# Optimization experiments

Hardware: AMD Instinct MI355X
Metric: run time of the kernel (lower is better)

## Reference

```python
import jax, jax.numpy as jnp
import numpy as np

NATTRS, NOBJS = 200, 500
N = NATTRS + NOBJS
E = 50000
IN_F, HID, NODE_D = 512, 2048, 512
IMG_D, EMB = 512, 800
B = 256


def _ln(x, g, b, eps=1e-5):
    mu = jnp.mean(x, axis=-1, keepdims=True)
    var = jnp.mean((x - mu) ** 2, axis=-1, keepdims=True)
    return (x - mu) * jax.lax.rsqrt(var + eps) * g + b


def _sage(x, src, dst, Wl, bl, Wr):
    # PyG SAGEConv: lin_l(mean_{j->i} x_j) + lin_r(x_i); lin_r has no bias.
    agg = jax.ops.segment_sum(x[src], dst, num_segments=x.shape[0])
    cnt = jax.ops.segment_sum(jnp.ones((src.shape[0],), x.dtype), dst, num_segments=x.shape[0])
    mean = agg / jnp.maximum(cnt, 1.0)[:, None]
    return mean @ Wl + bl + x @ Wr


def setup_inputs() -> dict:
    key = jax.random.key(0)
    ks = iter(jax.random.split(key, 40))
    rn = lambda shape, s=0.02: jax.random.normal(next(ks), shape, jnp.float32) * s
    inp = dict(
        img=jax.random.normal(next(ks), (B, IMG_D), jnp.float32),
        node_feats=jax.random.normal(next(ks), (N, IN_F), jnp.float32),
        edge_index=jax.random.randint(next(ks), (2, E), 0, N),
        # SAGEConv 1: in_f -> 2048
        s1_Wl=rn((IN_F, HID)), s1_bl=jnp.zeros((HID,), jnp.float32), s1_Wr=rn((IN_F, HID)),
        # SAGEConv 2: 2048 -> node_dim
        s2_Wl=rn((HID, NODE_D)), s2_bl=jnp.zeros((NODE_D,), jnp.float32), s2_Wr=rn((HID, NODE_D)),
        # img_fc: 512 -> 800 -> 1000 -> 800 (LayerNorm+ReLU hidden, LayerNorm output)
        i_W1=rn((IMG_D, 800)), i_b1=jnp.zeros((800,), jnp.float32), i_g1=jnp.ones((800,), jnp.float32), i_be1=jnp.zeros((800,), jnp.float32),
        i_W2=rn((800, 1000)), i_b2=jnp.zeros((1000,), jnp.float32), i_g2=jnp.ones((1000,), jnp.float32), i_be2=jnp.zeros((1000,), jnp.float32),
        i_W3=rn((1000, EMB)), i_b3=jnp.zeros((EMB,), jnp.float32), i_gn=jnp.ones((EMB,), jnp.float32), i_bn=jnp.zeros((EMB,), jnp.float32),
        # pair_fc: 1024 -> 1000 -> 800
        p_W1=rn((2 * NODE_D, 1000)), p_b1=jnp.zeros((1000,), jnp.float32), p_g1=jnp.ones((1000,), jnp.float32), p_be1=jnp.zeros((1000,), jnp.float32),
        p_W2=rn((1000, EMB)), p_b2=jnp.zeros((EMB,), jnp.float32), p_gn=jnp.ones((EMB,), jnp.float32), p_bn=jnp.zeros((EMB,), jnp.float32),
    )
    return inp


def reference(img, node_feats, edge_index,
              s1_Wl, s1_bl, s1_Wr, s2_Wl, s2_bl, s2_Wr,
              i_W1, i_b1, i_g1, i_be1, i_W2, i_b2, i_g2, i_be2, i_W3, i_b3, i_gn, i_bn,
              p_W1, p_b1, p_g1, p_be1, p_W2, p_b2, p_gn, p_bn):
    src, dst = edge_index[0], edge_index[1]
    # GAE.encode: SAGE -> ReLU -> (Dropout, eval=id) -> SAGE
    h = jax.nn.relu(_sage(node_feats, src, dst, s1_Wl, s1_bl, s1_Wr))
    nodes = _sage(h, src, dst, s2_Wl, s2_bl, s2_Wr)  # [N, node_dim]
    # img_fc
    t = jax.nn.relu(_ln(img @ i_W1 + i_b1, i_g1, i_be1))
    t = jax.nn.relu(_ln(t @ i_W2 + i_b2, i_g2, i_be2))
    img_feats = _ln(t @ i_W3 + i_b3, i_gn, i_bn)  # [B, EMB]
    # get_all_pairs (open-world cross product: attr repeated per obj, obj tiled)
    attr_nodes, obj_nodes = nodes[:NATTRS], nodes[NATTRS:]
    pairs = jnp.concatenate(
        [jnp.repeat(attr_nodes, NOBJS, axis=0), jnp.tile(obj_nodes, (NATTRS, 1))], axis=1)  # [P, 2*node_dim]
    u = jax.nn.relu(_ln(pairs @ p_W1 + p_b1, p_g1, p_be1))
    pair_nodes = _ln(u @ p_W2 + p_b2, p_gn, p_bn)  # [P, EMB]
    pair_pred = img_feats @ pair_nodes.T  # [B, P]
    return pair_pred, nodes
```

## Files before the change

### kernel.cpp

```cpp
#include <hip/hip_runtime.h>
#include <hip/hip_bf16.h>

#define NATTRS 200
#define NOBJS  500
#define NNODE  700
#define IN_F   512
#define HID    2048
#define NODE_D 512
#define IMG_D  512
#define EMB    800
#define BB     256
#define P_H1   1000
#define NPAIR  100000

typedef __attribute__((ext_vector_type(8))) short short8v;
typedef __attribute__((ext_vector_type(4))) float f32x4;

typedef const __attribute__((address_space(1))) unsigned int* gas_ptr;
typedef __attribute__((address_space(3))) unsigned int* las_ptr;
__device__ __forceinline__ void async_copy16(void* lds, const void* g) {
  __builtin_amdgcn_global_load_lds((gas_ptr)g, (las_ptr)lds, 16, 0, 0);
}

__device__ __forceinline__ ushort f2bf(float x) {
  __hip_bfloat16 b = __float2bfloat16(x);
  return *reinterpret_cast<ushort*>(&b);
}
__device__ __forceinline__ float bf2f(ushort u) {
  __hip_bfloat16 b;
  *reinterpret_cast<ushort*>(&b) = u;
  return __bfloat162float(b);
}

__global__ void k_count(const int* __restrict__ ei, int* __restrict__ cnt, int E) {
  int e = blockIdx.x * 256 + threadIdx.x;
  if (e < E) atomicAdd(&cnt[ei[E + e]], 1);
}

__global__ __launch_bounds__(1024) void k_scan(const int* __restrict__ cnt,
                                               int* __restrict__ row_start,
                                               int* __restrict__ pos) {
  __shared__ int s[1024];
  int t = threadIdx.x;
  int my = (t < NNODE) ? cnt[t] : 0;
  s[t] = my;
  __syncthreads();
  for (int off = 1; off < 1024; off <<= 1) {
    int add = (t >= off) ? s[t - off] : 0;
    __syncthreads();
    s[t] += add;
    __syncthreads();
  }
  int excl = s[t] - my;
  if (t < NNODE) { row_start[t] = excl; pos[t] = excl; }
  if (t == 0) row_start[NNODE] = s[1023];
}

__global__ void k_fill(const int* __restrict__ ei, int* __restrict__ pos,
                       int* __restrict__ srcs, int E) {
  int e = blockIdx.x * 256 + threadIdx.x;
  if (e < E) {
    int d = ei[E + e];
    int idx = atomicAdd(&pos[d], 1);
    srcs[idx] = ei[e];
  }
}

__global__ __launch_bounds__(256) void agg_mean(const float* __restrict__ X,
                                                const int* __restrict__ srcs,
                                                const int* __restrict__ row_start,
                                                float* __restrict__ outp, int D) {
  int node = blockIdx.x;
  int d = blockIdx.y * 256 + threadIdx.x;
  int e0 = row_start[node], e1 = row_start[node + 1];
  float s = 0.f;
  for (int e = e0; e < e1; ++e) s += X[srcs[e] * D + d];
  float c = (float)(e1 - e0);
  outp[node * D + d] = s / fmaxf(c, 1.f);
}

__global__ __launch_bounds__(256) void split_f32(const float* __restrict__ X,
                                                 ushort* __restrict__ Xh,
                                                 ushort* __restrict__ Xl,
                                                 int Mvalid, int K, int Kpad, long total) {
  for (long idx = blockIdx.x * 256L + threadIdx.x; idx < total; idx += gridDim.x * 256L) {
    int m = (int)(idx / Kpad);
    int k = (int)(idx - (long)m * Kpad);
    float v = (m < Mvalid && k < K) ? X[(size_t)m * K + k] : 0.f;
    ushort h = f2bf(v);
    Xh[idx] = h;
    Xl[idx] = f2bf(v - bf2f(h));
  }
}

struct WDesc { const float* W; ushort* Wh; ushort* Wl; int K, N, Kpad, nbx, blk0; };
struct WBatch { WDesc d[10]; };

__global__ __launch_bounds__(256) void prep_wT_batch(WBatch B) {
  __shared__ float tile[32][33];
  int bx = blockIdx.x;
  int di = 0;
  #pragma unroll
  for (int j = 1; j < 10; ++j) if (bx >= B.d[j].blk0) di = j;
  const WDesc& D = B.d[di];
  int local = bx - D.blk0;
  int bn = local % D.nbx, bk = local / D.nbx;
  const int n0 = bn * 32, k0 = bk * 32;
  const int tx = threadIdx.x & 31, ty = threadIdx.x >> 5;
  #pragma unroll
  for (int r0 = 0; r0 < 32; r0 += 8) {
    int k = k0 + r0 + ty, n = n0 + tx;
    tile[r0 + ty][tx] = (k < D.K && n < D.N) ? D.W[(size_t)k * D.N + n] : 0.f;
  }
  __syncthreads();
  #pragma unroll
  for (int r0 = 0; r0 < 32; r0 += 8) {
    int n = n0 + r0 + ty, kk = k0 + tx;
    float v = tile[tx][r0 + ty];
    ushort h = f2bf(v);
    D.Wh[(size_t)n * D.Kpad + kk] = h;
    D.Wl[(size_t)n * D.Kpad + kk] = f2bf(v - bf2f(h));
  }
}

__global__ __launch_bounds__(256) void w2rowsum(const float* __restrict__ W2,
                                                ushort* __restrict__ W2Th) {
  int k = blockIdx.x * 4 + (threadIdx.x >> 6);
  int lane = threadIdx.x & 63;
  const float* row = W2 + (size_t)k * EMB;
  float s = 0.f;
  for (int n = lane; n < EMB; n += 64) s += row[n];
  #pragma unroll
  for (int m = 1; m < 64; m <<= 1) s += __shfl_xor(s, m);
  if (lane == 0 && k < P_H1) W2Th[800 * 1024 + k] = f2bf(s);
}

template <bool RELU>
__global__ __launch_bounds__(256) void ln_rows(float* __restrict__ X,
                                               const float* __restrict__ g,
                                               const float* __restrict__ b, int N) {
  int row = blockIdx.x, tid = threadIdx.x;
  float* x = X + row * N;
  float s1 = 0.f, s2 = 0.f;
  for (int i = tid; i < N; i += 256) { float v = x[i]; s1 += v; s2 += v * v; }
  #pragma unroll
  for (int m = 1; m < 64; m <<= 1) { s1 += __shfl_xor(s1, m); s2 += __shfl_xor(s2, m); }
  __shared__ float r1[4], r2[4];
  int wv = tid >> 6;
  if ((tid & 63) == 0) { r1[wv] = s1; r2[wv] = s2; }
  __syncthreads();
  s1 = r1[0] + r1[1] + r1[2] + r1[3];
  s2 = r2[0] + r2[1] + r2[2] + r2[3];
  float inv = 1.f / (float)N;
  float mu = s1 * inv;
  float rstd = rsqrtf(s2 * inv - mu * mu + 1e-5f);
  for (int i = tid; i < N; i += 256) {
    float v = (x[i] - mu) * rstd * g[i] + b[i];
    if (RELU) v = fmaxf(v, 0.f);
    x[i] = v;
  }
}

__global__ __launch_bounds__(256) void prep_imgg(const float* __restrict__ t3,
                                                 const float* __restrict__ gn,
                                                 ushort* __restrict__ gh,
                                                 ushort* __restrict__ gl) {
  int r = blockIdx.x;
  for (int n = threadIdx.x; n < EMB; n += 256) {
    float v = t3[r * EMB + n] * gn[n];
    ushort h = f2bf(v);
    gh[r * EMB + n] = h;
    gl[r * EMB + n] = f2bf(v - bf2f(h));
  }
}

__global__ __launch_bounds__(256) void prep_pairB(const float* __restrict__ t3,
                                                  const float* __restrict__ gn,
                                                  const float* __restrict__ bn,
                                                  const float* __restrict__ b2,
                                                  float* __restrict__ Sv, float* __restrict__ Tv,
                                                  float* __restrict__ IBv, float* __restrict__ aux) {
  int b = blockIdx.x, tid = threadIdx.x;
  __shared__ float r1[4], r2[4], r3[4];
  float s1 = 0.f, s2 = 0.f, s3 = 0.f;
  if (b == BB) {
    for (int n = tid; n < EMB; n += 256) s1 += b2[n];
    #pragma unroll
    for (int m = 1; m < 64; m <<= 1) s1 += __shfl_xor(s1, m);
    if ((tid & 63) == 0) r1[tid >> 6] = s1;
    __syncthreads();
    if (tid == 0) aux[0] = (r1[0] + r1[1] + r1[2] + r1[3]) * (1.f / EMB);
    return;
  }
  const float* row = t3 + b * EMB;
  for (int n = tid; n < EMB; n += 256) {
    float iv = row[n];
    float ig = iv * gn[n];
    s1 += ig; s2 += iv * bn[n]; s3 += ig * b2[n];
  }
  #pragma unroll
  for (int m = 1; m < 64; m <<= 1) {
    s1 += __shfl_xor(s1, m); s2 += __shfl_xor(s2, m); s3 += __shfl_xor(s3, m);
  }
  int wv = tid >> 6;
  if ((tid & 63) == 0) { r1[wv] = s1; r2[wv] = s2; r3[wv] = s3; }
  __syncthreads();
  if (tid == 0) {
    Sv[b] = r1[0] + r1[1] + r1[2] + r1[3];
    Tv[b] = r2[0] + r2[1] + r2[2] + r2[3];
    IBv[b] = r3[0] + r3[1] + r3[2] + r3[3];
  }
}

__global__ __launch_bounds__(256) void ugen(const float* __restrict__ B1v,
                                            const float* __restrict__ O1v,
                                            const float* __restrict__ g1,
                                            const float* __restrict__ be1,
                                            ushort* __restrict__ Uh,
                                            ushort* __restrict__ Ul, int p0) {
  int r = blockIdx.x * 4 + (threadIdx.x >> 6);
  int lane = threadIdx.x & 63;
  int p = p0 + r;
  if (p > NPAIR - 1) p = NPAIR - 1;
  int a = p / NOBJS, o = p - a * NOBJS;
  const float* br = B1v + a * P_H1;
  const float* ow = O1v + o * P_H1;
  const int kb = lane * 16;
  float x[16];
  float s1 = 0.f, s2 = 0.f;
  #pragma unroll
  for (int i = 0; i < 16; ++i) {
    int k = kb + i;
    float v = (k < P_H1) ? br[k] + ow[k] : 0.f;
    x[i] = v; s1 += v; s2 += v * v;
  }
  #pragma unroll
  for (int m = 1; m < 64; m <<= 1) { s1 += __shfl_xor(s1, m); s2 += __shfl_xor(s2, m); }
  float mu = s1 * (1.f / P_H1);
  float rstd = rsqrtf(s2 * (1.f / P_H1) - mu * mu + 1e-5f);
  ushort hv[16], lv[16];
  #pragma unroll
  for (int i = 0; i < 16; ++i) {
    int k = kb + i;
    float un = (k < P_H1) ? fmaxf((x[i] - mu) * rstd * g1[k] + be1[k], 0.f) : 0.f;
    ushort h = f2bf(un);
    hv[i] = h;
    lv[i] = f2bf(un - bf2f(h));
  }
  size_t base = (size_t)r * 1024 + kb;
  *(short8v*)&Uh[base] = *(short8v*)&hv[0];
  *(short8v*)&Uh[base + 8] = *(short8v*)&hv[8];
  *(short8v*)&Ul[base] = *(short8v*)&lv[0];
  *(short8v*)&Ul[base + 8] = *(short8v*)&lv[8];
}

__global__ __launch_bounds__(256, 3) void ustat(const ushort* __restrict__ Uh,
                                                const ushort* __restrict__ W2Th,
                                                const float* __restrict__ b2,
                                                const float* __restrict__ aux,
                                                float* __restrict__ muv,
                                                float* __restrict__ rstdv) {
  __shared__ ushort smem[8192];
  __shared__ float red[2][128];
  const int tid = threadIdx.x, lane = tid & 63, wid = tid >> 6;
  const int wm = wid >> 1, wn = wid & 1;
  const int m0 = blockIdx.x * 128;
  const int lr = lane & 15, lk = lane >> 4;
  const int srow = lane >> 2;
  const int scol = (lane & 3) * 8;
  const float aux0 = aux[0];

  float ss[4][4] = {};
  float md[4][4] = {};

  for (int nt = 0; nt < 7; ++nt) {
    f32x4 acc[4][4];
    #pragma unroll
    for (int i = 0; i < 4; ++i)
      #pragma unroll
      for (int j = 0; j < 4; ++j) acc[i][j] = (f32x4){0.f, 0.f, 0.f, 0.f};

    for (int k0 = 0; k0 < 1024; k0 += 32) {
      __syncthreads();
      #pragma unroll
      for (int j = 0; j < 4; ++j) {
        int t = wid + 4 * j;
        int buf = t >> 3, i = t & 7;
        const ushort* src = buf == 0
            ? Uh + (size_t)(m0 + i * 16 + srow) * 1024 + k0 + scol
            : W2Th + (size_t)(nt * 128 + i * 16 + srow) * 1024 + k0 + scol;
        async_copy16(smem + buf * 4096 + i * 512, src);
      }
      __syncthreads();
      short8v ah[4], bh[4];
      #pragma unroll
      for (int f = 0; f < 4; ++f) {
        ah[f] = *(const short8v*)&smem[(wm * 64 + f * 16 + lr) * 32 + lk * 8];
        bh[f] = *(const short8v*)&smem[4096 + (wn * 64 + f * 16 + lr) * 32 + lk * 8];
      }
      #pragma unroll
      for (int mi = 0; mi < 4; ++mi)
        #pragma unroll
        for (int ni = 0; ni < 4; ++ni)
          acc[mi][ni] = __builtin_amdgcn_mfma_f32_16x16x32_bf16(ah[mi], bh[ni], acc[mi][ni], 0, 0, 0);
    }
    #pragma unroll
    for (int ni = 0; ni < 4; ++ni) {
      int n = nt * 128 + wn * 64 + ni * 16 + lr;
      if (n < EMB) {
        float bb = b2[n];
        #pragma unroll
        for (int mi = 0; mi < 4; ++mi)
          #pragma unroll
          for (int r = 0; r < 4; ++r) {
            float v = acc[mi][ni][r] + bb;
            ss[mi][r] += v * v;
          }
      } else if (n == EMB) {
        #pragma unroll
        for (int mi = 0; mi < 4; ++mi)
          #pragma unroll
          for (int r = 0; r < 4; ++r) md[mi][r] = acc[mi][ni][r];
      }
    }
  }
  #pragma unroll
  for (int mi = 0; mi < 4; ++mi)
    #pragma unroll
    for (int r = 0; r < 4; ++r) {
      float s = ss[mi][r];
      s += __shfl_xor(s, 1); s += __shfl_xor(s, 2);
      s += __shfl_xor(s, 4); s += __shfl_xor(s, 8);
      ss[mi][r] = s;
    }
  if (lr == 0) {
    #pragma unroll
    for (int mi = 0; mi < 4; ++mi)
      #pragma unroll
      for (int r = 0; r < 4; ++r)
        red[wn][wm * 64 + mi * 16 + lk * 4 + r] = ss[mi][r];
  }
  __syncthreads();
  if (wn == 0 && lr == 0) {
    #pragma unroll
    for (int mi = 0; mi < 4; ++mi)
      #pragma unroll
      for (int r = 0; r < 4; ++r) {
        int row = wm * 64 + mi * 16 + lk * 4 + r;
        float tot = red[0][row] + red[1][row];
        float m_ = md[mi][r] * (1.f / EMB) + aux0;
        muv[m0 + row] = m_;
        rstdv[m0 + row] = rsqrtf(tot * (1.f / EMB) - m_ * m_ + 1e-5f);
      }
  }
}

template <bool HAS2, bool HASBIAS, bool RELU, bool PAIREPI>
__global__ __launch_bounds__(256, 3) void gemm_mf(
    const ushort* __restrict__ Ah, const ushort* __restrict__ Al, int lda,
    const ushort* __restrict__ Bh, const ushort* __restrict__ Bl, int ldb,
    const ushort* __restrict__ A2h, const ushort* __restrict__ A2l, int lda2,
    const ushort* __restrict__ B2h, const ushort* __restrict__ B2l, int ldb2,
    const float* __restrict__ bias, float* __restrict__ C, size_t ldc,
    int K, int Mvalid, int nvalid, int ncol0,
    const float* __restrict__ rstdv, const float* __restrict__ muv,
    const float* __restrict__ Sv, const float* __restrict__ Tv,
    const float* __restrict__ IBv) {
  __shared__ ushort smem[16384];
  const int tid = threadIdx.x, lane = tid & 63, wid = tid >> 6;
  const int wm = wid >> 1, wn = wid & 1;
  const int n0b = blockIdx.x * 128, m0 = blockIdx.y * 128;
  const int lr = lane & 15, lk = lane >> 4;

  f32x4 acc[4][4];
  #pragma unroll
  for (int i = 0; i < 4; ++i)
    #pragma unroll
    for (int j = 0; j < 4; ++j) acc[i][j] = (f32x4){0.f, 0.f, 0.f, 0.f};

  const int srow = lane >> 2;
  const int scol = (lane & 3) * 8;
  const int npass = HAS2 ? 2 : 1;

  for (int pass = 0; pass < npass; ++pass) {
    const ushort* pAh = (HAS2 && pass) ? A2h : Ah;
    const ushort* pAl = (HAS2 && pass) ? A2l : Al;
    const ushort* pBh = (HAS2 && pass) ? B2h : Bh;
    const ushort* pBl = (HAS2 && pass) ? B2l : Bl;
    const int plda = (HAS2 && pass) ? lda2 : lda;
    const int pldb = (HAS2 && pass) ? ldb2 : ldb;

    for (int k0 = 0; k0 < K; k0 += 32) {
      __syncthreads();
      #pragma unroll
      for (int j = 0; j < 8; ++j) {
        int t = wid + 4 * j;
        int buf = t >> 3, i = t & 7;
        const ushort* g;
        int ld_, r0;
        if (buf == 0)      { g = pAh; ld_ = plda; r0 = m0; }
        else if (buf == 1) { g = pAl; ld_ = plda; r0 = m0; }
        else if (buf == 2) { g = pBh; ld_ = pldb; r0 = n0b; }
        else               { g = pBl; ld_ = pldb; r0 = n0b; }
        const ushort* src = g + (size_t)(r0 + i * 16 + srow) * ld_ + k0 + scol;
        async_copy16(smem + buf * 4096 + i * 512, src);
      }
      __syncthreads();

      short8v ah[4], al[4], bh[4], bl[4];
      #pragma unroll
      for (int f = 0; f < 4; ++f) {
        ah[f] = *(const short8v*)&smem[0     + (wm * 64 + f * 16 + lr) * 32 + lk * 8];
        al[f] = *(const short8v*)&smem[4096  + (wm * 64 + f * 16 + lr) * 32 + lk * 8];
        bh[f] = *(const short8v*)&smem[8192  + (wn * 64 + f * 16 + lr) * 32 + lk * 8];
        bl[f] = *(const short8v*)&smem[12288 + (wn * 64 + f * 16 + lr) * 32 + lk * 8];
      }
      #pragma unroll
      for (int mi = 0; mi < 4; ++mi)
        #pragma unroll
        for (int ni = 0; ni < 4; ++ni) {
          acc[mi][ni] = __builtin_amdgcn_mfma_f32_16x16x32_bf16(ah[mi], bh[ni], acc[mi][ni], 0, 0, 0);
          acc[mi][ni] = __builtin_amdgcn_mfma_f32_16x16x32_bf16(al[mi], bh[ni], acc[mi][ni], 0, 0, 0);
          acc[mi][ni] = __builtin_amdgcn_mfma_f32_16x16x32_bf16(ah[mi], bl[ni], acc[mi][ni], 0, 0, 0);
        }
    }
  }

  #pragma unroll
  for (int mi = 0; mi < 4; ++mi)
    #pragma unroll
    for (int ni = 0; ni < 4; ++ni) {
      int n = n0b + wn * 64 + ni * 16 + lr;
      if (n >= nvalid) continue;
      float rs = 0.f, mn = 0.f;
      if (PAIREPI) { rs = rstdv[n]; mn = muv[n]; }
      float bb = (HASBIAS && !PAIREPI) ? bias[n] : 0.f;
      #pragma unroll
      for (int r = 0; r < 4; ++r) {
        int m = m0 + wm * 64 + mi * 16 + lk * 4 + r;
        if (m >= Mvalid) continue;
        float v = acc[mi][ni][r];
        if (PAIREPI) {
          v = rs * (v + IBv[m] - mn * Sv[m]) + Tv[m];
        } else {
          v += bb;
          if (RELU) v = fmaxf(v, 0.f);
        }
        C[(size_t)m * ldc + ncol0 + n] = v;
      }
    }
}

extern "C" void kernel_launch(void* const* d_in, const int* in_sizes, int n_in,
                              void* d_out, int out_size, void* d_ws, size_t ws_size,
                              hipStream_t stream) {
  const float* img = (const float*)d_in[0];
  const float* node_feats = (const float*)d_in[1];
  const int* ei = (const int*)d_in[2];
  const float* s1_Wl = (const float*)d_in[3];
  const float* s1_bl = (const float*)d_in[4];
  const float* s1_Wr = (const float*)d_in[5];
  const float* s2_Wl = (const float*)d_in[6];
  const float* s2_bl = (const float*)d_in[7];
  const float* s2_Wr = (const float*)d_in[8];
  const float* i_W1 = (const float*)d_in[9];
  const float* i_b1 = (const float*)d_in[10];
  const float* i_g1 = (const float*)d_in[11];
  const float* i_be1 = (const float*)d_in[12];
  const float* i_W2 = (const float*)d_in[13];
  const float* i_b2 = (const float*)d_in[14];
  const float* i_g2 = (const float*)d_in[15];
  const float* i_be2 = (const float*)d_in[16];
  const float* i_W3 = (const float*)d_in[17];
  const float* i_b3 = (const float*)d_in[18];
  const float* i_gn = (const float*)d_in[19];
  const float* i_bn = (const float*)d_in[20];
  const float* p_W1 = (const float*)d_in[21];
  const float* p_b1 = (const float*)d_in[22];
  const float* p_g1 = (const float*)d_in[23];
  const float* p_be1 = (const float*)d_in[24];
  const float* p_W2 = (const float*)d_in[25];
  const float* p_b2 = (const float*)d_in[26];
  const float* p_gn = (const float*)d_in[27];
  const float* p_bn = (const float*)d_in[28];

  const int E = in_sizes[2] / 2;

  char* base = (char*)d_ws;
  size_t off = 0;
  auto alloc = [&](size_t bytes) -> void* {
    void* p = base + off;
    off = (off + bytes + 255) & ~(size_t)255;
    return p;
  };
  float* mean1 = (float*)alloc(700 * 512 * 4);
  float* h     = (float*)alloc(700 * 2048 * 4);
  float* mean2 = (float*)alloc(700 * 2048 * 4);
  float* t1    = (float*)alloc(256 * 800 * 4);
  float* t2    = (float*)alloc(256 * 1000 * 4);
  float* t3    = (float*)alloc(256 * 800 * 4);
  float* B1    = (float*)alloc(200 * 1000 * 4);
  float* O1    = (float*)alloc(500 * 1000 * 4);
  float* G     = (float*)alloc(256 * 1024 * 4);
  ushort* nfh = (ushort*)alloc(768 * 512 * 2);
  ushort* nfl = (ushort*)alloc(768 * 512 * 2);
  ushort* m1h = (ushort*)alloc(768 * 512 * 2);
  ushort* m1l = (ushort*)alloc(768 * 512 * 2);
  ushort* hh  = (ushort*)alloc(768 * 2048 * 2);
  ushort* hl  = (ushort*)alloc(768 * 2048 * 2);
  ushort* m2h = (ushort*)alloc(768 * 2048 * 2);
  ushort* m2l = (ushort*)alloc(768 * 2048 * 2);
  ushort* ndh = (ushort*)alloc(768 * 512 * 2);
  ushort* ndl = (ushort*)alloc(768 * 512 * 2);
  ushort* xih = (ushort*)alloc(256 * 512 * 2);
  ushort* xil = (ushort*)alloc(256 * 512 * 2);
  ushort* t1h = (ushort*)alloc(256 * 800 * 2);
  ushort* t1l = (ushort*)alloc(256 * 800 * 2);
  ushort* t2h = (ushort*)alloc(256 * 1024 * 2);
  ushort* t2l = (ushort*)alloc(256 * 1024 * 2);
  ushort* iggh = (ushort*)alloc(256 * 800 * 2);
  ushort* iggl = (ushort*)alloc(256 * 800 * 2);
  ushort* Gh   = (ushort*)alloc(256 * 1024 * 2);
  ushort* Gl   = (ushort*)alloc(256 * 1024 * 2);
  ushort* w1lh = (ushort*)alloc((size_t)2048 * 512 * 2);
  ushort* w1ll = (ushort*)alloc((size_t)2048 * 512 * 2);
  ushort* w1rh = (ushort*)alloc((size_t)2048 * 512 * 2);
  ushort* w1rl = (ushort*)alloc((size_t)2048 * 512 * 2);
  ushort* w2lh = (ushort*)alloc((size_t)512 * 2048 * 2);
  ushort* w2ll = (ushort*)alloc((size_t)512 * 2048 * 2);
  ushort* w2rh = (ushort*)alloc((size_t)512 * 2048 * 2);
  ushort* w2rl = (ushort*)alloc((size_t)512 * 2048 * 2);
  ushort* iw1h = (ushort*)alloc((size_t)896 * 512 * 2);
  ushort* iw1l = (ushort*)alloc((size_t)896 * 512 * 2);
  ushort* iw2h = (ushort*)alloc((size_t)1024 * 800 * 2);
  ushort* iw2l = (ushort*)alloc((size_t)1024 * 800 * 2);
  ushort* iw3h = (ushort*)alloc((size_t)896 * 1024 * 2);
  ushort* iw3l = (ushort*)alloc((size_t)896 * 1024 * 2);
  ushort* pw1ah = (ushort*)alloc((size_t)1024 * 512 * 2);
  ushort* pw1al = (ushort*)alloc((size_t)1024 * 512 * 2);
  ushort* pw1bh = (ushort*)alloc((size_t)1024 * 512 * 2);
  ushort* pw1bl = (ushort*)alloc((size_t)1024 * 512 * 2);
  ushort* W2Th = (ushort*)alloc((size_t)896 * 1024 * 2);
  ushort* W2Tl = (ushort*)alloc((size_t)896 * 1024 * 2);
  ushort* Wkh  = (ushort*)alloc((size_t)1024 * 800 * 2);
  ushort* Wkl  = (ushort*)alloc((size_t)1024 * 800 * 2);
  float* Sv  = (float*)alloc(256 * 4);
  float* Tv  = (float*)alloc(256 * 4);
  float* IBv = (float*)alloc(256 * 4);
  float* aux = (float*)alloc(256);
  int* cnt       = (int*)alloc(704 * 4);
  int* row_start = (int*)alloc(704 * 4);
  int* pos       = (int*)alloc(704 * 4);
  int* srcs      = (int*)alloc(50176 * 4);

  size_t avail = (ws_size > off + (4u << 20)) ? ws_size - off - (4u << 20) : 0;
  long maxRows = (long)(avail / 4104) - 256;
  int CA = (int)(maxRows / 500);
  if (CA < 1) CA = 1;
  if (CA > NATTRS) CA = NATTRS;
  int nch = (NATTRS + CA - 1) / CA;
  int rowsPadAlloc = ((CA * 500 + 127) / 128) * 128;
  ushort* Uh    = (ushort*)alloc((size_t)rowsPadAlloc * 1024 * 2);
  ushort* Ul    = (ushort*)alloc((size_t)rowsPadAlloc * 1024 * 2);
  float*  muv   = (float*)alloc((size_t)rowsPadAlloc * 4);
  float*  rstdv = (float*)alloc((size_t)rowsPadAlloc * 4);

  float* pairp = (float*)d_out;
  float* nodes = (float*)d_out + (size_t)BB * NPAIR;

  const ushort* NU = nullptr;
  const float* NUF = nullptr;

  hipMemsetAsync(cnt, 0, NNODE * sizeof(int), stream);
  k_count<<<(E + 255) / 256, 256, 0, stream>>>(ei, cnt, E);
  k_scan<<<1, 1024, 0, stream>>>(cnt, row_start, pos);
  k_fill<<<(E + 255) / 256, 256, 0, stream>>>(ei, pos, srcs, E);

  {
    WBatch B;
    int blk = 0;
    auto set = [&](int i, const float* W, ushort* Wh, ushort* Wl, int K, int N, int Kpad, int Npad) {
      B.d[i] = {W, Wh, Wl, K, N, Kpad, Npad / 32, blk};
      blk += (Npad / 32) * (Kpad / 32);
    };
    set(0, s1_Wl, w1lh, w1ll, 512, 2048, 512, 2048);
    set(1, s1_Wr, w1rh, w1rl, 512, 2048, 512, 2048);
    set(2, s2_Wl, w2lh, w2ll, 2048, 512, 2048, 512);
    set(3, s2_Wr, w2rh, w2rl, 2048, 512, 2048, 512);
    set(4, i_W1, iw1h, iw1l, 512, 800, 512, 896);
    set(5, i_W2, iw2h, iw2l, 800, 1000, 800, 1024);
    set(6, i_W3, iw3h, iw3l, 1000, 800, 1024, 896);
    set(7, p_W1, pw1ah, pw1al, 512, 1000, 512, 1024);
    set(8, p_W1 + 512 * 1000, pw1bh, pw1bl, 512, 1000, 512, 1024);
    set(9, p_W2, W2Th, W2Tl, 1000, 800, 1024, 896);
    prep_wT_batch<<<blk, 256, 0, stream>>>(B);
  }
  w2rowsum<<<250, 256, 0, stream>>>(p_W2, W2Th);
  split_f32<<<512, 256, 0, stream>>>(p_W2, Wkh, Wkl, 1000, 800, 800, 1024L * 800);

  agg_mean<<<dim3(NNODE, IN_F / 256), 256, 0, stream>>>(node_feats, srcs, row_start, mean1, IN_F);
  split_f32<<<512, 256, 0, stream>>>(node_feats, nfh, nfl, 700, 512, 512, 768L * 512);
  split_f32<<<512, 256, 0, stream>>>(mean1, m1h, m1l, 700, 512, 512, 768L * 512);
  gemm_mf<true, true, true, false><<<dim3(16, 6), 256, 0, stream>>>(
      m1h, m1l, 512, w1lh, w1ll, 512, nfh, nfl, 512, w1rh, w1rl, 512,
      s1_bl, h, 2048, 512, 700, 2048, 0, NUF, NUF, NUF, NUF, NUF);

  agg_mean<<<dim3(NNODE, HID / 256), 256, 0, stream>>>(h, srcs, row_start, mean2, HID);
  split_f32<<<1024, 256, 0, stream>>>(h, hh, hl, 700, 2048, 2048, 768L * 2048);
  split_f32<<<1024, 256, 0, stream>>>(mean2, m2h, m2l, 700, 2048, 2048, 768L * 2048);
  gemm_mf<true, true, false, false><<<dim3(4, 6), 256, 0, stream>>>(
      m2h, m2l, 2048, w2lh, w2ll, 2048, hh, hl, 2048, w2rh, w2rl, 2048,
      s2_bl, nodes, 512, 2048, 700, 512, 0, NUF, NUF, NUF, NUF, NUF);

  split_f32<<<256, 256, 0, stream>>>(img, xih, xil, 256, 512, 512, 256L * 512);
  gemm_mf<false, true, false, false><<<dim3(7, 2), 256, 0, stream>>>(
      xih, xil, 512, iw1h, iw1l, 512, NU, NU, 0, NU, NU, 0,
      i_b1, t1, 800, 512, 256, 800, 0, NUF, NUF, NUF, NUF, NUF);
  ln_rows<true><<<BB, 256, 0, stream>>>(t1, i_g1, i_be1, 800);
  split_f32<<<256, 256, 0, stream>>>(t1, t1h, t1l, 256, 800, 800, 256L * 800);
  gemm_mf<false, true, false, false><<<dim3(8, 2), 256, 0, stream>>>(
      t1h, t1l, 800, iw2h, iw2l, 800, NU, NU, 0, NU, NU, 0,
      i_b2, t2, 1000, 800, 256, 1000, 0, NUF, NUF, NUF, NUF, NUF);
  ln_rows<true><<<BB, 256, 0, stream>>>(t2, i_g2, i_be2, 1000);
  split_f32<<<256, 256, 0, stream>>>(t2, t2h, t2l, 256, 1000, 1024, 256L * 1024);
  gemm_mf<false, true, false, false><<<dim3(7, 2), 256, 0, stream>>>(
      t2h, t2l, 1024, iw3h, iw3l, 1024, NU, NU, 0, NU, NU, 0,
      i_b3, t3, 800, 1024, 256, 800, 0, NUF, NUF, NUF, NUF, NUF);
  ln_rows<false><<<BB, 256, 0, stream>>>(t3, i_gn, i_bn, EMB);

  prep_pairB<<<BB + 1, 256, 0, stream>>>(t3, p_gn, p_bn, p_b2, Sv, Tv, IBv, aux);
  prep_imgg<<<BB, 256, 0, stream>>>(t3, p_gn, iggh, iggl);
  gemm_mf<false, false, false, false><<<dim3(8, 2), 256, 0, stream>>>(
      iggh, iggl, 800, Wkh, Wkl, 800, NU, NU, 0, NU, NU, 0,
      nullptr, G, 1024, 800, 256, 1024, 0, NUF, NUF, NUF, NUF, NUF);
  split_f32<<<256, 256, 0, stream>>>(G, Gh, Gl, 256, 1024, 1024, 256L * 1024);

  split_f32<<<512, 256, 0, stream>>>(nodes, ndh, ndl, 700, 512, 512, 768L * 512);
  gemm_mf<false, true, false, false><<<dim3(8, 2), 256, 0, stream>>>(
      ndh, ndl, 512, pw1ah, pw1al, 512, NU, NU, 0, NU, NU, 0,
      p_b1, B1, 1000, 512, 200, 1000, 0, NUF, NUF, NUF, NUF, NUF);
  gemm_mf<false, false, false, false><<<dim3(8, 4), 256, 0, stream>>>(
      ndh + 200 * 512, ndl + 200 * 512, 512, pw1bh, pw1bl, 512, NU, NU, 0, NU, NU, 0,
      nullptr, O1, 1000, 512, 500, 1000, 0, NUF, NUF, NUF, NUF, NUF);

  for (int c = 0; c < nch; ++c) {
    int a0 = c * CA;
    int ca = (NATTRS - a0 < CA) ? (NATTRS - a0) : CA;
    int rows = ca * 500;
    int rowsPad = ((rows + 127) / 128) * 128;
    int p0 = a0 * 500;

    ugen<<<rowsPad / 4, 256, 0, stream>>>(B1, O1, p_g1, p_be1, Uh, Ul, p0);
    ustat<<<rowsPad / 128, 256, 0, stream>>>(Uh, W2Th, p_b2, aux, muv, rstdv);
    gemm_mf<false, false, false, true><<<dim3(rowsPad / 128, 2), 256, 0, stream>>>(
        Gh, Gl, 1024, Uh, Ul, 1024, NU, NU, 0, NU, NU, 0,
        nullptr, pairp, NPAIR, 1024, 256, rows, p0,
        rstdv, muv, Sv, Tv, IBv);
  }
}
```

Before: 2.134 ms.

## Fuse pair-hidden generation into stat and output GEMMs, drop materialized U buffer

Stops writing the 100000x1024 pair hidden matrix U (hi/lo bf16) to global memory and rebuilds each tile on the fly inside the stat and output GEMM kernels from B1/O1 rows. Per-pair layer-norm mean and variance come from precomputed row sums plus a small B1·O1ᵀ dot-product GEMM, which removes the per-pair reduction and the chunked launch loop. It also fuses LayerNorm with the bf16 split for the image MLP. The cost is redundant recomputation of U elements in each GEMM block (twice across the two N-tiles of the output kernel) plus scalar global loads in the inner loop, and the variance formula is less numerically stable.

```diff
diff --git a/kernel.cpp b/kernel.cpp
--- a/kernel.cpp
+++ b/kernel.cpp
@@ -12,6 +12,7 @@
 #define BB     256
 #define P_H1   1000
 #define NPAIR  100000
+#define NPB    782
 
 typedef __attribute__((ext_vector_type(8))) short short8v;
 typedef __attribute__((ext_vector_type(4))) float f32x4;
@@ -82,11 +83,12 @@
 __global__ __launch_bounds__(256) void split_f32(const float* __restrict__ X,
                                                  ushort* __restrict__ Xh,
                                                  ushort* __restrict__ Xl,
-                                                 int Mvalid, int K, int Kpad, long total) {
+                                                 int Mvalid, int K, int ldx, int Kpad,
+                                                 long total) {
   for (long idx = blockIdx.x * 256L + threadIdx.x; idx < total; idx += gridDim.x * 256L) {
     int m = (int)(idx / Kpad);
     int k = (int)(idx - (long)m * Kpad);
-    float v = (m < Mvalid && k < K) ? X[(size_t)m * K + k] : 0.f;
+    float v = (m < Mvalid && k < K) ? X[(size_t)m * ldx + k] : 0.f;
     ushort h = f2bf(v);
     Xh[idx] = h;
     Xl[idx] = f2bf(v - bf2f(h));
@@ -133,6 +135,21 @@
   #pragma unroll
   for (int m = 1; m < 64; m <<= 1) s += __shfl_xor(s, m);
   if (lane == 0 && k < P_H1) W2Th[800 * 1024 + k] = f2bf(s);
+}
+
+__global__ __launch_bounds__(256) void rowstats(const float* __restrict__ B1v,
+                                                const float* __restrict__ O1v,
+                                                float* __restrict__ s1v,
+                                                float* __restrict__ s2v) {
+  int row = blockIdx.x * 4 + (threadIdx.x >> 6);
+  int lane = threadIdx.x & 63;
+  const float* ptr = (row < 200) ? B1v + (size_t)row * 1024
+                                 : O1v + (size_t)(row - 200) * 1024;
+  float s1 = 0.f, s2 = 0.f;
+  for (int k = lane; k < P_H1; k += 64) { float v = ptr[k]; s1 += v; s2 += v * v; }
+  #pragma unroll
+  for (int m = 1; m < 64; m <<= 1) { s1 += __shfl_xor(s1, m); s2 += __shfl_xor(s2, m); }
+  if (lane == 0 && row < 700) { s1v[row] = s1; s2v[row] = s2; }
 }
 
 template <bool RELU>
@@ -161,6 +178,40 @@
   }
 }
 
+template <bool RELU>
+__global__ __launch_bounds__(256) void ln_split(const float* __restrict__ X,
+                                                const float* __restrict__ g,
+                                                const float* __restrict__ b,
+                                                ushort* __restrict__ Xh,
+                                                ushort* __restrict__ Xl,
+                                                int N, int Kpad) {
+  int row = blockIdx.x, tid = threadIdx.x;
+  const float* x = X + (size_t)row * N;
+  float s1 = 0.f, s2 = 0.f;
+  for (int i = tid; i < N; i += 256) { float v = x[i]; s1 += v; s2 += v * v; }
+  #pragma unroll
+  for (int m = 1; m < 64; m <<= 1) { s1 += __shfl_xor(s1, m); s2 += __shfl_xor(s2, m); }
+  __shared__ float r1[4], r2[4];
+  int wv = tid >> 6;
+  if ((tid & 63) == 0) { r1[wv] = s1; r2[wv] = s2; }
+  __syncthreads();
+  s1 = r1[0] + r1[1] + r1[2] + r1[3];
+  s2 = r2[0] + r2[1] + r2[2] + r2[3];
+  float inv = 1.f / (float)N;
+  float mu = s1 * inv;
+  float rstd = rsqrtf(s2 * inv - mu * mu + 1e-5f);
+  for (int i = tid; i < Kpad; i += 256) {
+    float v = 0.f;
+    if (i < N) {
+      v = (x[i] - mu) * rstd * g[i] + b[i];
+      if (RELU) v = fmaxf(v, 0.f);
+    }
+    ushort h = f2bf(v);
+    Xh[(size_t)row * Kpad + i] = h;
+    Xl[(size_t)row * Kpad + i] = f2bf(v - bf2f(h));
+  }
+}
+
 __global__ __launch_bounds__(256) void prep_imgg(const float* __restrict__ t3,
                                                  const float* __restrict__ gn,
                                                  ushort* __restrict__ gh,
@@ -212,63 +263,33 @@
   }
 }
 
-__global__ __launch_bounds__(256) void ugen(const float* __restrict__ B1v,
-                                            const float* __restrict__ O1v,
-                                            const float* __restrict__ g1,
-                                            const float* __restrict__ be1,
-                                            ushort* __restrict__ Uh,
-                                            ushort* __restrict__ Ul, int p0) {
-  int r = blockIdx.x * 4 + (threadIdx.x >> 6);
-  int lane = threadIdx.x & 63;
-  int p = p0 + r;
-  if (p > NPAIR - 1) p = NPAIR - 1;
-  int a = p / NOBJS, o = p - a * NOBJS;
-  const float* br = B1v + a * P_H1;
-  const float* ow = O1v + o * P_H1;
-  const int kb = lane * 16;
-  float x[16];
-  float s1 = 0.f, s2 = 0.f;
-  #pragma unroll
-  for (int i = 0; i < 16; ++i) {
-    int k = kb + i;
-    float v = (k < P_H1) ? br[k] + ow[k] : 0.f;
-    x[i] = v; s1 += v; s2 += v * v;
-  }
-  #pragma unroll
-  for (int m = 1; m < 64; m <<= 1) { s1 += __shfl_xor(s1, m); s2 += __shfl_xor(s2, m); }
-  float mu = s1 * (1.f / P_H1);
-  float rstd = rsqrtf(s2 * (1.f / P_H1) - mu * mu + 1e-5f);
-  ushort hv[16], lv[16];
-  #pragma unroll
-  for (int i = 0; i < 16; ++i) {
-    int k = kb + i;
-    float un = (k < P_H1) ? fmaxf((x[i] - mu) * rstd * g1[k] + be1[k], 0.f) : 0.f;
-    ushort h = f2bf(un);
-    hv[i] = h;
-    lv[i] = f2bf(un - bf2f(h));
-  }
-  size_t base = (size_t)r * 1024 + kb;
-  *(short8v*)&Uh[base] = *(short8v*)&hv[0];
-  *(short8v*)&Uh[base + 8] = *(short8v*)&hv[8];
-  *(short8v*)&Ul[base] = *(short8v*)&lv[0];
-  *(short8v*)&Ul[base + 8] = *(short8v*)&lv[8];
-}
-
-__global__ __launch_bounds__(256, 3) void ustat(const ushort* __restrict__ Uh,
-                                                const ushort* __restrict__ W2Th,
-                                                const float* __restrict__ b2,
-                                                const float* __restrict__ aux,
-                                                float* __restrict__ muv,
-                                                float* __restrict__ rstdv) {
+__global__ __launch_bounds__(256, 3) void fused_ustat(
+    const float* __restrict__ B1v, const float* __restrict__ O1v,
+    const float* __restrict__ g1, const float* __restrict__ be1,
+    const float* __restrict__ s1v, const float* __restrict__ s2v,
+    const float* __restrict__ dotBO,
+    const ushort* __restrict__ W2Th, const float* __restrict__ b2,
+    const float* __restrict__ aux,
+    float* __restrict__ muv, float* __restrict__ rstdv) {
   __shared__ ushort smem[8192];
   __shared__ float red[2][128];
   const int tid = threadIdx.x, lane = tid & 63, wid = tid >> 6;
   const int wm = wid >> 1, wn = wid & 1;
   const int m0 = blockIdx.x * 128;
   const int lr = lane & 15, lk = lane >> 4;
-  const int srow = lane >> 2;
-  const int scol = (lane & 3) * 8;
+  const int srow = lane >> 2, scol = (lane & 3) * 8;
   const float aux0 = aux[0];
+
+  const int rr = tid >> 1, ch = tid & 1;
+  int p = m0 + rr;
+  if (p > NPAIR - 1) p = NPAIR - 1;
+  const int a = p / NOBJS, o = p - a * NOBJS;
+  const float* pB = B1v + (size_t)a * 1024;
+  const float* pO = O1v + (size_t)o * 1024;
+  const float s1p = s1v[a] + s1v[200 + o];
+  const float s2p = s2v[a] + 2.f * dotBO[a * 512 + o] + s2v[200 + o];
+  const float mu1 = s1p * (1.f / P_H1);
+  const float rstd1 = rsqrtf(s2p * (1.f / P_H1) - mu1 * mu1 + 1e-5f);
 
   float ss[4][4] = {};
   float md[4][4] = {};
@@ -283,13 +304,24 @@
     for (int k0 = 0; k0 < 1024; k0 += 32) {
       __syncthreads();
       #pragma unroll
-      for (int j = 0; j < 4; ++j) {
-        int t = wid + 4 * j;
-        int buf = t >> 3, i = t & 7;
-        const ushort* src = buf == 0
-            ? Uh + (size_t)(m0 + i * 16 + srow) * 1024 + k0 + scol
-            : W2Th + (size_t)(nt * 128 + i * 16 + srow) * 1024 + k0 + scol;
-        async_copy16(smem + buf * 4096 + i * 512, src);
+      for (int j = 0; j < 2; ++j) {
+        int i = wid + 4 * j;
+        const ushort* src = W2Th + (size_t)(nt * 128 + i * 16 + srow) * 1024 + k0 + scol;
+        async_copy16(smem + 4096 + i * 512, src);
+      }
+      {
+        const int kb = k0 + ch * 16;
+        ushort hv[16];
+        #pragma unroll
+        for (int i = 0; i < 16; ++i) {
+          int k = kb + i;
+          float un = 0.f;
+          if (k < P_H1)
+            un = fmaxf((pB[k] + pO[k] - mu1) * rstd1 * g1[k] + be1[k], 0.f);
+          hv[i] = f2bf(un);
+        }
+        *(short8v*)&smem[rr * 32 + ch * 16] = *(short8v*)&hv[0];
+        *(short8v*)&smem[rr * 32 + ch * 16 + 8] = *(short8v*)&hv[8];
       }
       __syncthreads();
       short8v ah[4], bh[4];
@@ -355,17 +387,112 @@
   }
 }
 
-template <bool HAS2, bool HASBIAS, bool RELU, bool PAIREPI>
+__global__ __launch_bounds__(256, 3) void fused_out(
+    const ushort* __restrict__ Gh, const ushort* __restrict__ Gl,
+    const float* __restrict__ B1v, const float* __restrict__ O1v,
+    const float* __restrict__ g1, const float* __restrict__ be1,
+    const float* __restrict__ s1v, const float* __restrict__ s2v,
+    const float* __restrict__ dotBO,
+    float* __restrict__ C,
+    const float* __restrict__ rstdv, const float* __restrict__ muv,
+    const float* __restrict__ Sv, const float* __restrict__ Tv,
+    const float* __restrict__ IBv) {
+  __shared__ ushort smem[16384];
+  const int tid = threadIdx.x, lane = tid & 63, wid = tid >> 6;
+  const int wm = wid >> 1, wn = wid & 1;
+  const int n0b = blockIdx.x * 128, m0 = blockIdx.y * 128;
+  const int lr = lane & 15, lk = lane >> 4;
+  const int srow = lane >> 2, scol = (lane & 3) * 8;
+
+  const int rr = tid >> 1, ch = tid & 1;
+  int p = n0b + rr;
+  if (p > NPAIR - 1) p = NPAIR - 1;
+  const int a = p / NOBJS, o = p - a * NOBJS;
+  const float* pB = B1v + (size_t)a * 1024;
+  const float* pO = O1v + (size_t)o * 1024;
+  const float s1p = s1v[a] + s1v[200 + o];
+  const float s2p = s2v[a] + 2.f * dotBO[a * 512 + o] + s2v[200 + o];
+  const float mu1 = s1p * (1.f / P_H1);
+  const float rstd1 = rsqrtf(s2p * (1.f / P_H1) - mu1 * mu1 + 1e-5f);
+
+  f32x4 acc[4][4];
+  #pragma unroll
+  for (int i = 0; i < 4; ++i)
+    #pragma unroll
+    for (int j = 0; j < 4; ++j) acc[i][j] = (f32x4){0.f, 0.f, 0.f, 0.f};
+
+  for (int k0 = 0; k0 < 1024; k0 += 32) {
+    __syncthreads();
+    #pragma unroll
+    for (int j = 0; j < 4; ++j) {
+      int t = wid + 4 * j;
+      int buf = t >> 3, i = t & 7;
+      const ushort* g = buf ? Gl : Gh;
+      const ushort* src = g + (size_t)(m0 + i * 16 + srow) * 1024 + k0 + scol;
+      async_copy16(smem + buf * 4096 + i * 512, src);
+    }
+    {
+      const int kb = k0 + ch * 16;
+      ushort hv[16], lv[16];
+      #pragma unroll
+      for (int i = 0; i < 16; ++i) {
+        int k = kb + i;
+        float un = 0.f;
+        if (k < P_H1)
+          un = fmaxf((pB[k] + pO[k] - mu1) * rstd1 * g1[k] + be1[k], 0.f);
+        ushort h = f2bf(un);
+        hv[i] = h;
+        lv[i] = f2bf(un - bf2f(h));
+      }
+      *(short8v*)&smem[8192 + rr * 32 + ch * 16] = *(short8v*)&hv[0];
+      *(short8v*)&smem[8192 + rr * 32 + ch * 16 + 8] = *(short8v*)&hv[8];
+      *(short8v*)&smem[12288 + rr * 32 + ch * 16] = *(short8v*)&lv[0];
+      *(short8v*)&smem[12288 + rr * 32 + ch * 16 + 8] = *(short8v*)&lv[8];
+    }
+    __syncthreads();
+
+    short8v ah[4], al[4], bh[4], bl[4];
+    #pragma unroll
+    for (int f = 0; f < 4; ++f) {
+      ah[f] = *(const short8v*)&smem[0     + (wm * 64 + f * 16 + lr) * 32 + lk * 8];
+      al[f] = *(const short8v*)&smem[4096  + (wm * 64 + f * 16 + lr) * 32 + lk * 8];
+      bh[f] = *(const short8v*)&smem[8192  + (wn * 64 + f * 16 + lr) * 32 + lk * 8];
+      bl[f] = *(const short8v*)&smem[12288 + (wn * 64 + f * 16 + lr) * 32 + lk * 8];
+    }
+    #pragma unroll
+    for (int mi = 0; mi < 4; ++mi)
+      #pragma unroll
+      for (int ni = 0; ni < 4; ++ni) {
+        acc[mi][ni] = __builtin_amdgcn_mfma_f32_16x16x32_bf16(ah[mi], bh[ni], acc[mi][ni], 0, 0, 0);
+        acc[mi][ni] = __builtin_amdgcn_mfma_f32_16x16x32_bf16(al[mi], bh[ni], acc[mi][ni], 0, 0, 0);
+        acc[mi][ni] = __builtin_amdgcn_mfma_f32_16x16x32_bf16(ah[mi], bl[ni], acc[mi][ni], 0, 0, 0);
+      }
+  }
+
+  #pragma unroll
+  for (int mi = 0; mi < 4; ++mi)
+    #pragma unroll
+    for (int ni = 0; ni < 4; ++ni) {
+      int n = n0b + wn * 64 + ni * 16 + lr;
+      if (n >= NPAIR) continue;
+      float rs = rstdv[n], mn = muv[n];
+      #pragma unroll
+      for (int r = 0; r < 4; ++r) {
+        int m = m0 + wm * 64 + mi * 16 + lk * 4 + r;
+        float v = acc[mi][ni][r];
+        C[(size_t)m * NPAIR + n] = rs * (v + IBv[m] - mn * Sv[m]) + Tv[m];
+      }
+    }
+}
+
+template <bool HAS2, bool HASBIAS, bool RELU>
 __global__ __launch_bounds__(256, 3) void gemm_mf(
     const ushort* __restrict__ Ah, const ushort* __restrict__ Al, int lda,
     const ushort* __restrict__ Bh, const ushort* __restrict__ Bl, int ldb,
     const ushort* __restrict__ A2h, const ushort* __restrict__ A2l, int lda2,
     const ushort* __restrict__ B2h, const ushort* __restrict__ B2l, int ldb2,
     const float* __restrict__ bias, float* __restrict__ C, size_t ldc,
-    int K, int Mvalid, int nvalid, int ncol0,
-    const float* __restrict__ rstdv, const float* __restrict__ muv,
-    const float* __restrict__ Sv, const float* __restrict__ Tv,
-    const float* __restrict__ IBv) {
+    int K, int Mvalid, int nvalid, int ncol0) {
   __shared__ ushort smem[16384];
   const int tid = threadIdx.x, lane = tid & 63, wid = tid >> 6;
   const int wm = wid >> 1, wn = wid & 1;
@@ -432,20 +559,13 @@
     for (int ni = 0; ni < 4; ++ni) {
       int n = n0b + wn * 64 + ni * 16 + lr;
       if (n >= nvalid) continue;
-      float rs = 0.f, mn = 0.f;
-      if (PAIREPI) { rs = rstdv[n]; mn = muv[n]; }
-      float bb = (HASBIAS && !PAIREPI) ? bias[n] : 0.f;
+      float bb = HASBIAS ? bias[n] : 0.f;
       #pragma unroll
       for (int r = 0; r < 4; ++r) {
         int m = m0 + wm * 64 + mi * 16 + lk * 4 + r;
         if (m >= Mvalid) continue;
-        float v = acc[mi][ni][r];
-        if (PAIREPI) {
-          v = rs * (v + IBv[m] - mn * Sv[m]) + Tv[m];
-        } else {
-          v += bb;
-          if (RELU) v = fmaxf(v, 0.f);
-        }
+        float v = acc[mi][ni][r] + bb;
+        if (RELU) v = fmaxf(v, 0.f);
         C[(size_t)m * ldc + ncol0 + n] = v;
       }
     }
@@ -499,9 +619,10 @@
   float* t1    = (float*)alloc(256 * 800 * 4);
   float* t2    = (float*)alloc(256 * 1000 * 4);
   float* t3    = (float*)alloc(256 * 800 * 4);
-  float* B1    = (float*)alloc(200 * 1000 * 4);
-  float* O1    = (float*)alloc(500 * 1000 * 4);
+  float* B1    = (float*)alloc(256 * 1024 * 4);
+  float* O1    = (float*)alloc(512 * 1024 * 4);
   float* G     = (float*)alloc(256 * 1024 * 4);
+  float* dotBO = (float*)alloc(256 * 512 * 4);
   ushort* nfh = (ushort*)alloc(768 * 512 * 2);
   ushort* nfl = (ushort*)alloc(768 * 512 * 2);
   ushort* m1h = (ushort*)alloc(768 * 512 * 2);
@@ -522,6 +643,10 @@
   ushort* iggl = (ushort*)alloc(256 * 800 * 2);
   ushort* Gh   = (ushort*)alloc(256 * 1024 * 2);
   ushort* Gl   = (ushort*)alloc(256 * 1024 * 2);
+  ushort* B1h  = (ushort*)alloc(256 * 1024 * 2);
+  ushort* B1l  = (ushort*)alloc(256 * 1024 * 2);
+  ushort* O1h  = (ushort*)alloc(512 * 1024 * 2);
+  ushort* O1l  = (ushort*)alloc(512 * 1024 * 2);
   ushort* w1lh = (ushort*)alloc((size_t)2048 * 512 * 2);
   ushort* w1ll = (ushort*)alloc((size_t)2048 * 512 * 2);
   ushort* w1rh = (ushort*)alloc((size_t)2048 * 512 * 2);
@@ -548,28 +673,19 @@
   float* Tv  = (float*)alloc(256 * 4);
   float* IBv = (float*)alloc(256 * 4);
   float* aux = (float*)alloc(256);
+  float* s1v = (float*)alloc(704 * 4);
+  float* s2v = (float*)alloc(704 * 4);
+  float* muv   = (float*)alloc((size_t)NPB * 128 * 4);
+  float* rstdv = (float*)alloc((size_t)NPB * 128 * 4);
   int* cnt       = (int*)alloc(704 * 4);
   int* row_start = (int*)alloc(704 * 4);
   int* pos       = (int*)alloc(704 * 4);
   int* srcs      = (int*)alloc(50176 * 4);
 
-  size_t avail = (ws_size > off + (4u << 20)) ? ws_size - off - (4u << 20) : 0;
-  long maxRows = (long)(avail / 4104) - 256;
-  int CA = (int)(maxRows / 500);
-  if (CA < 1) CA = 1;
-  if (CA > NATTRS) CA = NATTRS;
-  int nch = (NATTRS + CA - 1) / CA;
-  int rowsPadAlloc = ((CA * 500 + 127) / 128) * 128;
-  ushort* Uh    = (ushort*)alloc((size_t)rowsPadAlloc * 1024 * 2);
-  ushort* Ul    = (ushort*)alloc((size_t)rowsPadAlloc * 1024 * 2);
-  float*  muv   = (float*)alloc((size_t)rowsPadAlloc * 4);
-  float*  rstdv = (float*)alloc((size_t)rowsPadAlloc * 4);
-
   float* pairp = (float*)d_out;
   float* nodes = (float*)d_out + (size_t)BB * NPAIR;
 
   const ushort* NU = nullptr;
-  const float* NUF = nullptr;
 
   hipMemsetAsync(cnt, 0, NNODE * sizeof(int), stream);
   k_count<<<(E + 255) / 256, 256, 0, stream>>>(ei, cnt, E);
@@ -596,65 +712,61 @@
     prep_wT_batch<<<blk, 256, 0, stream>>>(B);
   }
   w2rowsum<<<250, 256, 0, stream>>>(p_W2, W2Th);
-  split_f32<<<512, 256, 0, stream>>>(p_W2, Wkh, Wkl, 1000, 800, 800, 1024L * 800);
+  split_f32<<<512, 256, 0, stream>>>(p_W2, Wkh, Wkl, 1000, 800, 800, 800, 1024L * 800);
 
   agg_mean<<<dim3(NNODE, IN_F / 256), 256, 0, stream>>>(node_feats, srcs, row_start, mean1, IN_F);
-  split_f32<<<512, 256, 0, stream>>>(node_feats, nfh, nfl, 700, 512, 512, 768L * 512);
-  split_f32<<<512, 256, 0, stream>>>(mean1, m1h, m1l, 700, 512, 512, 768L * 512);
-  gemm_mf<true, true, true, false><<<dim3(16, 6), 256, 0, stream>>>(
+  split_f32<<<512, 256, 0, stream>>>(node_feats, nfh, nfl, 700, 512, 512, 512, 768L * 512);
+  split_f32<<<512, 256, 0, stream>>>(mean1, m1h, m1l, 700, 512, 512, 512, 768L * 512);
+  gemm_mf<true, true, true><<<dim3(16, 6), 256, 0, stream>>>(
       m1h, m1l, 512, w1lh, w1ll, 512, nfh, nfl, 512, w1rh, w1rl, 512,
-      s1_bl, h, 2048, 512, 700, 2048, 0, NUF, NUF, NUF, NUF, NUF);
+      s1_bl, h, 2048, 512, 700, 2048, 0);
 
   agg_mean<<<dim3(NNODE, HID / 256), 256, 0, stream>>>(h, srcs, row_start, mean2, HID);
-  split_f32<<<1024, 256, 0, stream>>>(h, hh, hl, 700, 2048, 2048, 768L * 2048);
-  split_f32<<<1024, 256, 0, stream>>>(mean2, m2h, m2l, 700, 2048, 2048, 768L * 2048);
-  gemm_mf<true, true, false, false><<<dim3(4, 6), 256, 0, stream>>>(
+  split_f32<<<1024, 256, 0, stream>>>(h, hh, hl, 700, 2048, 2048, 2048, 768L * 2048);
+  split_f32<<<1024, 256, 0, stream>>>(mean2, m2h, m2l, 700, 2048, 2048, 2048, 768L * 2048);
+  gemm_mf<true, true, false><<<dim3(4, 6), 256, 0, stream>>>(
       m2h, m2l, 2048, w2lh, w2ll, 2048, hh, hl, 2048, w2rh, w2rl, 2048,
-      s2_bl, nodes, 512, 2048, 700, 512, 0, NUF, NUF, NUF, NUF, NUF);
-
-  split_f32<<<256, 256, 0, stream>>>(img, xih, xil, 256, 512, 512, 256L * 512);
-  gemm_mf<false, true, false, false><<<dim3(7, 2), 256, 0, stream>>>(
+      s2_bl, nodes, 512, 2048, 700, 512, 0);
+
+  split_f32<<<256, 256, 0, stream>>>(img, xih, xil, 256, 512, 512, 512, 256L * 512);
+  gemm_mf<false, true, false><<<dim3(7, 2), 256, 0, stream>>>(
       xih, xil, 512, iw1h, iw1l, 512, NU, NU, 0, NU, NU, 0,
-      i_b1, t1, 800, 512, 256, 800, 0, NUF, NUF, NUF, NUF, NUF);
-  ln_rows<true><<<BB, 256, 0, stream>>>(t1, i_g1, i_be1, 800);
-  split_f32<<<256, 256, 0, stream>>>(t1, t1h, t1l, 256, 800, 800, 256L * 800);
-  gemm_mf<false, true, false, false><<<dim3(8, 2), 256, 0, stream>>>(
+      i_b1, t1, 800, 512, 256, 800, 0);
+  ln_split<true><<<BB, 256, 0, stream>>>(t1, i_g1, i_be1, t1h, t1l, 800, 800);
+  gemm_mf<false, true, false><<<dim3(8, 2), 256, 0, stream>>>(
       t1h, t1l, 800, iw2h, iw2l, 800, NU, NU, 0, NU, NU, 0,
-      i_b2, t2, 1000, 800, 256, 1000, 0, NUF, NUF, NUF, NUF, NUF);
-  ln_rows<true><<<BB, 256, 0, stream>>>(t2, i_g2, i_be2, 1000);
-  split_f32<<<256, 256, 0, stream>>>(t2, t2h, t2l, 256, 1000, 1024, 256L * 1024);
-  gemm_mf<false, true, false, false><<<dim3(7, 2), 256, 0, stream>>>(
+      i_b2, t2, 1000, 800, 256, 1000, 0);
+  ln_split<true><<<BB, 256, 0, stream>>>(t2, i_g2, i_be2, t2h, t2l, 1000, 1024);
+  gemm_mf<false, true, false><<<dim3(7, 2), 256, 0, stream>>>(
       t2h, t2l, 1024, iw3h, iw3l, 1024, NU, NU, 0, NU, NU, 0,
-      i_b3, t3, 800, 1024, 256, 800, 0, NUF, NUF, NUF, NUF, NUF);
+      i_b3, t3, 800, 1024, 256, 800, 0);
   ln_rows<false><<<BB, 256, 0, stream>>>(t3, i_gn, i_bn, EMB);
 
   prep_pairB<<<BB + 1, 256, 0, stream>>>(t3, p_gn, p_bn, p_b2, Sv, Tv, IBv, aux);
   prep_imgg<<<BB, 256, 0, stream>>>(t3, p_gn, iggh, iggl);
-  gemm_mf<false, false, false, false><<<dim3(8, 2), 256, 0, stream>>>(
+  gemm_mf<false, false, false><<<dim3(8, 2), 256, 0, stream>>>(
       iggh, iggl, 800, Wkh, Wkl, 800, NU, NU, 0, NU, NU, 0,
-      nullptr, G, 1024, 800, 256, 1024, 0, NUF, NUF, NUF, NUF, NUF);
-  split_f32<<<256, 256, 0, stream>>>(G, Gh, Gl, 256, 1024, 1024, 256L * 1024);
-
-  split_f32<<<512, 256, 0, stream>>>(nodes, ndh, ndl, 700, 512, 512, 768L * 512);
-  gemm_mf<false, true, false, false><<<dim3(8, 2), 256, 0, stream>>>(
+      nullptr, G, 1024, 800, 256, 1024, 0);
+  split_f32<<<256, 256, 0, stream>>>(G, Gh, Gl, 256, 1024, 1024, 1024, 256L * 1024);
+
+  split_f32<<<512, 256, 0, stream>>>(nodes, ndh, ndl, 700, 512, 512, 512, 768L * 512);
+  gemm_mf<false, true, false><<<dim3(8, 2), 256, 0, stream>>>(
       ndh, ndl, 512, pw1ah, pw1al, 512, NU, NU, 0, NU, NU, 0,
-      p_b1, B1, 1000, 512, 200, 1000, 0, NUF, NUF, NUF, NUF, NUF);
-  gemm_mf<false, false, false, false><<<dim3(8, 4), 256, 0, stream>>>(
+      p_b1, B1, 1024, 512, 200, 1000, 0);
+  gemm_mf<false, false, false><<<dim3(8, 4), 256, 0, stream>>>(
       ndh + 200 * 512, ndl + 200 * 512, 512, pw1bh, pw1bl, 512, NU, NU, 0, NU, NU, 0,
-      nullptr, O1, 1000, 512, 500, 1000, 0, NUF, NUF, NUF, NUF, NUF);
-
-  for (int c = 0; c < nch; ++c) {
-    int a0 = c * CA;
-    int ca = (NATTRS - a0 < CA) ? (NATTRS - a0) : CA;
-    int rows = ca * 500;
-    int rowsPad = ((rows + 127) / 128) * 128;
-    int p0 = a0 * 500;
-
-    ugen<<<rowsPad / 4, 256, 0, stream>>>(B1, O1, p_g1, p_be1, Uh, Ul, p0);
-    ustat<<<rowsPad / 128, 256, 0, stream>>>(Uh, W2Th, p_b2, aux, muv, rstdv);
-    gemm_mf<false, false, false, true><<<dim3(rowsPad / 128, 2), 256, 0, stream>>>(
-        Gh, Gl, 1024, Uh, Ul, 1024, NU, NU, 0, NU, NU, 0,
-        nullptr, pairp, NPAIR, 1024, 256, rows, p0,
-        rstdv, muv, Sv, Tv, IBv);
-  }
-}
+      nullptr, O1, 1024, 512, 500, 1000, 0);
+
+  rowstats<<<175, 256, 0, stream>>>(B1, O1, s1v, s2v);
+  split_f32<<<512, 256, 0, stream>>>(B1, B1h, B1l, 200, 1000, 1024, 1024, 256L * 1024);
+  split_f32<<<512, 256, 0, stream>>>(O1, O1h, O1l, 500, 1000, 1024, 1024, 512L * 1024);
+  gemm_mf<false, false, false><<<dim3(4, 2), 256, 0, stream>>>(
+      B1h, B1l, 1024, O1h, O1l, 1024, NU, NU, 0, NU, NU, 0,
+      nullptr, dotBO, 512, 1024, 200, 500, 0);
+
+  fused_ustat<<<NPB, 256, 0, stream>>>(B1, O1, p_g1, p_be1, s1v, s2v, dotBO,
+                                       W2Th, p_b2, aux, muv, rstdv);
+  fused_out<<<dim3(NPB, 2), 256, 0, stream>>>(Gh, Gl, B1, O1, p_g1, p_be1,
+                                              s1v, s2v, dotBO, pairp,
+                                              rstdv, muv, Sv, Tv, IBv);
+}
```

Measured after the change: 4.377 ms. 2.05x slower.
